# Performance work log

Measured on AMD Instinct MI355X. Metric: run time of the kernel, lower is better.

Reference implementation:

```python
import jax, jax.numpy as jnp
import numpy as np

EPS = 1e-9
LAMBDA_VIOLATION = 0.5

B, S, K, N, M = 2048, 20, 128, 256, 10  # batch, num_samples, k, n, m


def setup_inputs() -> dict:
    key = jax.random.key(0)
    k1, k2, k3, k4 = jax.random.split(key, 4)
    y_pred = jax.random.uniform(k1, (B, 1), dtype=jnp.float32) * 10.0 + 1.0
    y_true = jax.random.uniform(k2, (B, 1), dtype=jnp.float32) * 10.0 + 1.0
    P_padded = jax.random.normal(k3, (B, K, N - K), dtype=jnp.float32)
    samples = jax.random.normal(k4, (B, S, K), dtype=jnp.float32)
    return {"y_pred": y_pred, "y_true": y_true, "P_padded": P_padded,
            "samples": samples, "m": M}


def reference(y_pred, y_true, P_padded, samples, m):
    b, s, k = samples.shape
    n = k + P_padded.shape[2]
    # LogMSE term
    yp = jnp.clip(y_pred, EPS)
    yt = jnp.clip(y_true, EPS)
    logmse = jnp.mean((jnp.log2(yt) - jnp.log2(yp)) ** 2)
    # Build generator matrices G = [I_k | P] : [B, k, n]
    I = jnp.broadcast_to(jnp.eye(k, dtype=P_padded.dtype), (b, k, k))
    G = jnp.concatenate([I, P_padded], axis=2)
    # Random codewords: [B, S, n]
    codewords = jnp.einsum('bsk,bkn->bsn', samples, G)
    mags = jnp.abs(codewords).reshape(b * s, n)
    top_vals, _ = jax.lax.top_k(mags, m + 1)  # [B*S, m+1] descending
    hm = (top_vals[:, 0] / (top_vals[:, m] + EPS)).reshape(b, s)
    max_hm = jnp.max(hm, axis=1)  # [B]
    penalty = jnp.sum(jax.nn.relu(max_hm - y_pred.squeeze(-1)))
    violation = penalty / b
    total_loss = logmse + LAMBDA_VIOLATION * violation
    return total_loss, logmse, violation
```

## Files before the change

kernel.cpp:

```cpp
#include <hip/hip_runtime.h>
#include <math.h>

#define EPSF 1e-9f
#define KK 128
#define MTOP 10

__global__ __launch_bounds__(256, 4) void fused_kernel(
    const float* __restrict__ y_pred, const float* __restrict__ y_true,
    const float* __restrict__ P, const float* __restrict__ samples,
    float* __restrict__ partial )
{
    const int tid   = threadIdx.x;
    const int wave  = tid >> 6;
    const int lane  = tid & 63;
    const int b     = blockIdx.x;
    const int r0    = wave * 5;
    const int sg    = lane >> 5;
    const int c     = lane & 31;
    const int j4    = c << 2;
    const int kbase = sg << 6;

    const float* __restrict__ Pb = P + ((size_t)b << 14);
    const float* __restrict__ Sb = samples + (size_t)b * (20 * KK);

    __shared__ float sS[20 * KK];
    __shared__ float red[4];

#pragma unroll
    for (int i = 0; i < 5; ++i) {
        const int idx = (i * 256 + tid) * 2;
        *(float2*)&sS[idx] = *(const float2*)(Sb + idx);
    }
    __syncthreads();

    float4 acc[5];
#pragma unroll
    for (int r = 0; r < 5; ++r) acc[r] = make_float4(0.f, 0.f, 0.f, 0.f);

    const float* __restrict__ Pw = Pb + (size_t)kbase * KK + j4;
#pragma unroll 2
    for (int kk = 0; kk < 64; kk += 4) {
        float4 p0 = *(const float4*)(Pw + (kk + 0) * KK);
        float4 p1 = *(const float4*)(Pw + (kk + 1) * KK);
        float4 p2 = *(const float4*)(Pw + (kk + 2) * KK);
        float4 p3 = *(const float4*)(Pw + (kk + 3) * KK);
#pragma unroll
        for (int r = 0; r < 5; ++r) {
            float4 s = *(const float4*)&sS[(r0 + r) * KK + kbase + kk];
            acc[r].x = fmaf(s.x, p0.x, acc[r].x);
            acc[r].y = fmaf(s.x, p0.y, acc[r].y);
            acc[r].z = fmaf(s.x, p0.z, acc[r].z);
            acc[r].w = fmaf(s.x, p0.w, acc[r].w);
            acc[r].x = fmaf(s.y, p1.x, acc[r].x);
            acc[r].y = fmaf(s.y, p1.y, acc[r].y);
            acc[r].z = fmaf(s.y, p1.z, acc[r].z);
            acc[r].w = fmaf(s.y, p1.w, acc[r].w);
            acc[r].x = fmaf(s.z, p2.x, acc[r].x);
            acc[r].y = fmaf(s.z, p2.y, acc[r].y);
            acc[r].z = fmaf(s.z, p2.z, acc[r].z);
            acc[r].w = fmaf(s.z, p2.w, acc[r].w);
            acc[r].x = fmaf(s.w, p3.x, acc[r].x);
            acc[r].y = fmaf(s.w, p3.y, acc[r].y);
            acc[r].z = fmaf(s.w, p3.z, acc[r].z);
            acc[r].w = fmaf(s.w, p3.w, acc[r].w);
        }
    }

    float w0[5], w1[5], w2[5], w3[5];
#pragma unroll
    for (int r = 0; r < 5; ++r) {
        float ax = acc[r].x + __shfl_xor(acc[r].x, 32, 64);
        float ay = acc[r].y + __shfl_xor(acc[r].y, 32, 64);
        float az = acc[r].z + __shfl_xor(acc[r].z, 32, 64);
        float aw = acc[r].w + __shfl_xor(acc[r].w, 32, 64);
        float4 idv = *(const float4*)&sS[(r0 + r) * KK + j4];
        w0[r] = fabsf(sg ? idv.x : ax);
        w1[r] = fabsf(sg ? idv.y : ay);
        w2[r] = fabsf(sg ? idv.z : az);
        w3[r] = fabsf(sg ? idv.w : aw);
    }

    float mx[5];
#pragma unroll
    for (int r = 0; r < 5; ++r) {
        float lm = fmaxf(fmaxf(w0[r], w1[r]), fmaxf(w2[r], w3[r]));
#pragma unroll
        for (int d = 32; d >= 1; d >>= 1)
            lm = fmaxf(lm, __shfl_xor(lm, d, 64));
        mx[r] = lm;
    }

    unsigned lo[5], hi[5];
#pragma unroll
    for (int r = 0; r < 5; ++r) { lo[r] = 0u; hi[r] = __float_as_uint(mx[r]); }

    while (lo[0] < hi[0] || lo[1] < hi[1] || lo[2] < hi[2] ||
           lo[3] < hi[3] || lo[4] < hi[4]) {
#pragma unroll
        for (int r = 0; r < 5; ++r) {
            unsigned mid = lo[r] + ((hi[r] - lo[r] + 1u) >> 1);
            float mf = __uint_as_float(mid);
            int cnt = __popcll(__ballot(w0[r] > mf)) + __popcll(__ballot(w1[r] > mf))
                    + __popcll(__ballot(w2[r] > mf)) + __popcll(__ballot(w3[r] > mf));
            bool g = cnt >= (MTOP + 1);
            lo[r] = g ? mid : lo[r];
            hi[r] = g ? hi[r] : mid - 1u;
        }
    }

    float hmax = 0.f;
#pragma unroll
    for (int r = 0; r < 5; ++r) {
        float m11 = __uint_as_float(lo[r] + 1u);
        hmax = fmaxf(hmax, mx[r] / (m11 + EPSF));
    }

    if (lane == 0) red[wave] = hmax;
    __syncthreads();
    if (tid == 0) {
        float hb  = fmaxf(fmaxf(red[0], red[1]), fmaxf(red[2], red[3]));
        float ypv = y_pred[b];
        float yp  = fmaxf(ypv, EPSF);
        float yt  = fmaxf(y_true[b], EPSF);
        float d   = log2f(yt) - log2f(yp);
        partial[2 * b]     = d * d;
        partial[2 * b + 1] = fmaxf(hb - ypv, 0.f);
    }
}

__global__ __launch_bounds__(256) void finalize_kernel(
    const float* __restrict__ partial, float* __restrict__ out, float invB)
{
    const int t = threadIdx.x;
    float sl = 0.f, sp = 0.f;
#pragma unroll
    for (int i = 0; i < 8; ++i) {
        float2 v = *(const float2*)(partial + 2 * (t + i * 256));
        sl += v.x; sp += v.y;
    }
#pragma unroll
    for (int d = 32; d >= 1; d >>= 1) {
        sl += __shfl_xor(sl, d, 64);
        sp += __shfl_xor(sp, d, 64);
    }
    __shared__ float rl[4], rp[4];
    const int w = t >> 6;
    if ((t & 63) == 0) { rl[w] = sl; rp[w] = sp; }
    __syncthreads();
    if (t == 0) {
        float L = (rl[0] + rl[1] + rl[2] + rl[3]) * invB;
        float V = (rp[0] + rp[1] + rp[2] + rp[3]) * invB;
        out[0] = L + 0.5f * V;
        out[1] = L;
        out[2] = V;
    }
}

extern "C" void kernel_launch(void* const* d_in, const int* in_sizes, int n_in,
                              void* d_out, int out_size, void* d_ws, size_t ws_size,
                              hipStream_t stream) {
    const float* y_pred  = (const float*)d_in[0];
    const float* y_true  = (const float*)d_in[1];
    const float* P       = (const float*)d_in[2];
    const float* samples = (const float*)d_in[3];
    const int B = in_sizes[0];

    float* partial = (float*)d_ws;

    fused_kernel<<<B, 256, 0, stream>>>(y_pred, y_true, P, samples, partial);
    finalize_kernel<<<1, 256, 0, stream>>>(partial, (float*)d_out, 1.0f / (float)B);
}
```

Measured before the change: 235.9 us.

## Split each batch into two 128-thread blocks with swizzled mapping and prefetch

Each batch element is now handled by two 128-thread blocks, each doing 10 of the 20 sample rows, so the grid has twice as many smaller blocks. Block indices are swizzled so the two halves of a batch element land apart, and the P loads are software-prefetched one step ahead of the FMA loop. The log-MSE and penalty math moves into the finalize kernel, which also merges the two half maxima. The aim is better occupancy and latency hiding, but P for each batch is now read by two blocks, doubling its global traffic unless the cache serves it.

Result: slower. 260.0 us (+10.2%).

```diff
diff --git a/kernel.cpp b/kernel.cpp
--- a/kernel.cpp
+++ b/kernel.cpp
@@ -5,31 +5,39 @@
 #define KK 128
 #define MTOP 10
 
-__global__ __launch_bounds__(256, 4) void fused_kernel(
-    const float* __restrict__ y_pred, const float* __restrict__ y_true,
+__global__ __launch_bounds__(128, 7) void fused_kernel(
     const float* __restrict__ P, const float* __restrict__ samples,
-    float* __restrict__ partial )
+    float* __restrict__ hq )
 {
-    const int tid   = threadIdx.x;
-    const int wave  = tid >> 6;
-    const int lane  = tid & 63;
-    const int b     = blockIdx.x;
-    const int r0    = wave * 5;
-    const int sg    = lane >> 5;
-    const int c     = lane & 31;
-    const int j4    = c << 2;
+    const int tid  = threadIdx.x;
+    const int wave = tid >> 6;
+    const int lane = tid & 63;
+
+    const int u = blockIdx.x;
+    int b, h;
+    if ((gridDim.x & 15) == 0) {
+        const int perx = gridDim.x >> 4;
+        b = (u & 7) * perx + (u >> 4);
+        h = (u >> 3) & 1;
+    } else {
+        b = u >> 1;
+        h = u & 1;
+    }
+    const int q  = h * 2 + wave;
+    const int sg = lane >> 5;
+    const int c  = lane & 31;
+    const int j4 = c << 2;
     const int kbase = sg << 6;
 
-    const float* __restrict__ Pb = P + ((size_t)b << 14);
-    const float* __restrict__ Sb = samples + (size_t)b * (20 * KK);
+    __shared__ float sS[2 * 5 * KK];
+    __shared__ float redh[2];
+    float* __restrict__ sW = sS + wave * (5 * KK);
 
-    __shared__ float sS[20 * KK];
-    __shared__ float red[4];
-
+    const float* __restrict__ Sb = samples + ((size_t)b * 20 + q * 5) * KK;
 #pragma unroll
     for (int i = 0; i < 5; ++i) {
-        const int idx = (i * 256 + tid) * 2;
-        *(float2*)&sS[idx] = *(const float2*)(Sb + idx);
+        const int idx = i * KK + lane * 2;
+        *(float2*)&sW[idx] = *(const float2*)(Sb + idx);
     }
     __syncthreads();
 
@@ -37,16 +45,25 @@
 #pragma unroll
     for (int r = 0; r < 5; ++r) acc[r] = make_float4(0.f, 0.f, 0.f, 0.f);
 
-    const float* __restrict__ Pw = Pb + (size_t)kbase * KK + j4;
-#pragma unroll 2
+    const float* __restrict__ Pw = P + ((size_t)b << 14) + (size_t)kbase * KK + j4;
+    float4 p0 = *(const float4*)(Pw + 0 * KK);
+    float4 p1 = *(const float4*)(Pw + 1 * KK);
+    float4 p2 = *(const float4*)(Pw + 2 * KK);
+    float4 p3 = *(const float4*)(Pw + 3 * KK);
+#pragma unroll
     for (int kk = 0; kk < 64; kk += 4) {
-        float4 p0 = *(const float4*)(Pw + (kk + 0) * KK);
-        float4 p1 = *(const float4*)(Pw + (kk + 1) * KK);
-        float4 p2 = *(const float4*)(Pw + (kk + 2) * KK);
-        float4 p3 = *(const float4*)(Pw + (kk + 3) * KK);
+        float4 q0, q1, q2, q3;
+        const bool pf = (kk + 4) < 64;
+        if (pf) {
+            const float* Pn = Pw + (size_t)(kk + 4) * KK;
+            q0 = *(const float4*)(Pn + 0 * KK);
+            q1 = *(const float4*)(Pn + 1 * KK);
+            q2 = *(const float4*)(Pn + 2 * KK);
+            q3 = *(const float4*)(Pn + 3 * KK);
+        }
 #pragma unroll
         for (int r = 0; r < 5; ++r) {
-            float4 s = *(const float4*)&sS[(r0 + r) * KK + kbase + kk];
+            float4 s = *(const float4*)&sW[r * KK + kbase + kk];
             acc[r].x = fmaf(s.x, p0.x, acc[r].x);
             acc[r].y = fmaf(s.x, p0.y, acc[r].y);
             acc[r].z = fmaf(s.x, p0.z, acc[r].z);
@@ -64,6 +81,7 @@
             acc[r].z = fmaf(s.w, p3.z, acc[r].z);
             acc[r].w = fmaf(s.w, p3.w, acc[r].w);
         }
+        if (pf) { p0 = q0; p1 = q1; p2 = q2; p3 = q3; }
     }
 
     float w0[5], w1[5], w2[5], w3[5];
@@ -73,7 +91,7 @@
         float ay = acc[r].y + __shfl_xor(acc[r].y, 32, 64);
         float az = acc[r].z + __shfl_xor(acc[r].z, 32, 64);
         float aw = acc[r].w + __shfl_xor(acc[r].w, 32, 64);
-        float4 idv = *(const float4*)&sS[(r0 + r) * KK + j4];
+        float4 idv = *(const float4*)&sW[r * KK + j4];
         w0[r] = fabsf(sg ? idv.x : ax);
         w1[r] = fabsf(sg ? idv.y : ay);
         w2[r] = fabsf(sg ? idv.z : az);
@@ -115,28 +133,27 @@
         hmax = fmaxf(hmax, mx[r] / (m11 + EPSF));
     }
 
-    if (lane == 0) red[wave] = hmax;
+    if (lane == 0) redh[wave] = hmax;
     __syncthreads();
-    if (tid == 0) {
-        float hb  = fmaxf(fmaxf(red[0], red[1]), fmaxf(red[2], red[3]));
-        float ypv = y_pred[b];
-        float yp  = fmaxf(ypv, EPSF);
-        float yt  = fmaxf(y_true[b], EPSF);
-        float d   = log2f(yt) - log2f(yp);
-        partial[2 * b]     = d * d;
-        partial[2 * b + 1] = fmaxf(hb - ypv, 0.f);
-    }
+    if (tid == 0) hq[2 * b + h] = fmaxf(redh[0], redh[1]);
 }
 
 __global__ __launch_bounds__(256) void finalize_kernel(
-    const float* __restrict__ partial, float* __restrict__ out, float invB)
+    const float* __restrict__ hq, const float* __restrict__ y_pred,
+    const float* __restrict__ y_true, float* __restrict__ out,
+    float invB, int B)
 {
     const int t = threadIdx.x;
     float sl = 0.f, sp = 0.f;
-#pragma unroll
-    for (int i = 0; i < 8; ++i) {
-        float2 v = *(const float2*)(partial + 2 * (t + i * 256));
-        sl += v.x; sp += v.y;
+    for (int bb = t; bb < B; bb += 256) {
+        float2 h2 = *(const float2*)(hq + 2 * bb);
+        float hb  = fmaxf(h2.x, h2.y);
+        float ypv = y_pred[bb];
+        float yp  = fmaxf(ypv, EPSF);
+        float yt  = fmaxf(y_true[bb], EPSF);
+        float d   = log2f(yt) - log2f(yp);
+        sl += d * d;
+        sp += fmaxf(hb - ypv, 0.f);
     }
 #pragma unroll
     for (int d = 32; d >= 1; d >>= 1) {
@@ -165,8 +182,9 @@
     const float* samples = (const float*)d_in[3];
     const int B = in_sizes[0];
 
-    float* partial = (float*)d_ws;
+    float* hq = (float*)d_ws;
 
-    fused_kernel<<<B, 256, 0, stream>>>(y_pred, y_true, P, samples, partial);
-    finalize_kernel<<<1, 256, 0, stream>>>(partial, (float*)d_out, 1.0f / (float)B);
+    fused_kernel<<<2 * B, 128, 0, stream>>>(P, samples, hq);
+    finalize_kernel<<<1, 256, 0, stream>>>(hq, y_pred, y_true, (float*)d_out,
+                                           1.0f / (float)B, B);
 }
```

## Stage P through double-buffered LDS with async global_load_lds pipeline

Applied to the files above, without the earlier changes.

Replaces direct per-thread global loads of the P matrix with asynchronous global-to-LDS copies via global_load_lds into a two-stage shared buffer. Each of eight chunks is prefetched while the previous chunk is consumed, so memory latency overlaps the FMA work. The occupancy hint rises from 4 to 6 blocks per CU. The cost is 16 KB of extra LDS per block, a barrier per chunk, and correctness that depends on the async-copy lane-to-address mapping and on no wait for outstanding vmcnt before the barrier.

After: 232.1 us. About the same (-1.6%).

```diff
diff --git a/kernel.cpp b/kernel.cpp
--- a/kernel.cpp
+++ b/kernel.cpp
@@ -5,7 +5,48 @@
 #define KK 128
 #define MTOP 10
 
-__global__ __launch_bounds__(256, 4) void fused_kernel(
+
+#define GLDS16(G, L) __builtin_amdgcn_global_load_lds(                    \
+    (const __attribute__((address_space(1))) void*)(G),                   \
+    (__attribute__((address_space(3))) void*)(L), 16, 0, 0)
+
+#define STAGE_ISSUE(T, BUF, I)                                            \
+    GLDS16(Pb + (size_t)(((T) << 3) + rowoff + (wave << 2) + ((I) << 1)   \
+                         + l5) * KK + (lx << 2),                          \
+           &sP[BUF][((wave << 2) + ((I) << 1)) * KK])
+#define STAGE_CHUNK(T, BUF) { STAGE_ISSUE(T, BUF, 0); STAGE_ISSUE(T, BUF, 1); }
+
+#define FMA5G(T, BUF, G)                                                  \
+    {                                                                     \
+        const float* pbse = &sP[BUF][((sg << 3) + ((G) << 2)) * KK + j4]; \
+        float4 p0 = *(const float4*)(pbse + 0 * KK);                      \
+        float4 p1 = *(const float4*)(pbse + 1 * KK);                      \
+        float4 p2 = *(const float4*)(pbse + 2 * KK);                      \
+        float4 p3 = *(const float4*)(pbse + 3 * KK);                      \
+        const int soff = kbase + ((T) << 3) + ((G) << 2);                 \
+        _Pragma("unroll")                                                 \
+        for (int r = 0; r < 5; ++r) {                                     \
+            float4 s = *(const float4*)&sS[(r0 + r) * KK + soff];         \
+            acc[r].x = fmaf(s.x, p0.x, acc[r].x);                         \
+            acc[r].y = fmaf(s.x, p0.y, acc[r].y);                         \
+            acc[r].z = fmaf(s.x, p0.z, acc[r].z);                         \
+            acc[r].w = fmaf(s.x, p0.w, acc[r].w);                         \
+            acc[r].x = fmaf(s.y, p1.x, acc[r].x);                         \
+            acc[r].y = fmaf(s.y, p1.y, acc[r].y);                         \
+            acc[r].z = fmaf(s.y, p1.z, acc[r].z);                         \
+            acc[r].w = fmaf(s.y, p1.w, acc[r].w);                         \
+            acc[r].x = fmaf(s.z, p2.x, acc[r].x);                         \
+            acc[r].y = fmaf(s.z, p2.y, acc[r].y);                         \
+            acc[r].z = fmaf(s.z, p2.z, acc[r].z);                         \
+            acc[r].w = fmaf(s.z, p2.w, acc[r].w);                         \
+            acc[r].x = fmaf(s.w, p3.x, acc[r].x);                         \
+            acc[r].y = fmaf(s.w, p3.y, acc[r].y);                         \
+            acc[r].z = fmaf(s.w, p3.z, acc[r].z);                         \
+            acc[r].w = fmaf(s.w, p3.w, acc[r].w);                         \
+        }                                                                 \
+    }
+
+__global__ __launch_bounds__(256, 6) void fused_kernel(
     const float* __restrict__ y_pred, const float* __restrict__ y_true,
     const float* __restrict__ P, const float* __restrict__ samples,
     float* __restrict__ partial )
@@ -19,11 +60,15 @@
     const int c     = lane & 31;
     const int j4    = c << 2;
     const int kbase = sg << 6;
+    const int l5    = lane >> 5;
+    const int lx    = lane & 31;
+    const int rowoff = (wave >= 2) ? 56 : 0;
 
     const float* __restrict__ Pb = P + ((size_t)b << 14);
     const float* __restrict__ Sb = samples + (size_t)b * (20 * KK);
 
     __shared__ float sS[20 * KK];
+    __shared__ float sP[2][16 * KK];
     __shared__ float red[4];
 
 #pragma unroll
@@ -31,40 +76,25 @@
         const int idx = (i * 256 + tid) * 2;
         *(float2*)&sS[idx] = *(const float2*)(Sb + idx);
     }
+
+    float4 acc[5];
+#pragma unroll
+    for (int r = 0; r < 5; ++r) acc[r] = make_float4(0.f, 0.f, 0.f, 0.f);
+
+    STAGE_CHUNK(0, 0);
     __syncthreads();
 
-    float4 acc[5];
-#pragma unroll
-    for (int r = 0; r < 5; ++r) acc[r] = make_float4(0.f, 0.f, 0.f, 0.f);
-
-    const float* __restrict__ Pw = Pb + (size_t)kbase * KK + j4;
-#pragma unroll 2
-    for (int kk = 0; kk < 64; kk += 4) {
-        float4 p0 = *(const float4*)(Pw + (kk + 0) * KK);
-        float4 p1 = *(const float4*)(Pw + (kk + 1) * KK);
-        float4 p2 = *(const float4*)(Pw + (kk + 2) * KK);
-        float4 p3 = *(const float4*)(Pw + (kk + 3) * KK);
-#pragma unroll
-        for (int r = 0; r < 5; ++r) {
-            float4 s = *(const float4*)&sS[(r0 + r) * KK + kbase + kk];
-            acc[r].x = fmaf(s.x, p0.x, acc[r].x);
-            acc[r].y = fmaf(s.x, p0.y, acc[r].y);
-            acc[r].z = fmaf(s.x, p0.z, acc[r].z);
-            acc[r].w = fmaf(s.x, p0.w, acc[r].w);
-            acc[r].x = fmaf(s.y, p1.x, acc[r].x);
-            acc[r].y = fmaf(s.y, p1.y, acc[r].y);
-            acc[r].z = fmaf(s.y, p1.z, acc[r].z);
-            acc[r].w = fmaf(s.y, p1.w, acc[r].w);
-            acc[r].x = fmaf(s.z, p2.x, acc[r].x);
-            acc[r].y = fmaf(s.z, p2.y, acc[r].y);
-            acc[r].z = fmaf(s.z, p2.z, acc[r].z);
-            acc[r].w = fmaf(s.z, p2.w, acc[r].w);
-            acc[r].x = fmaf(s.w, p3.x, acc[r].x);
-            acc[r].y = fmaf(s.w, p3.y, acc[r].y);
-            acc[r].z = fmaf(s.w, p3.z, acc[r].z);
-            acc[r].w = fmaf(s.w, p3.w, acc[r].w);
-        }
-    }
+    int cur = 0;
+#pragma unroll 1
+    for (int t = 0; t < 7; ++t) {
+        STAGE_CHUNK(t + 1, cur ^ 1);
+        FMA5G(t, cur, 0)
+        FMA5G(t, cur, 1)
+        __syncthreads();
+        cur ^= 1;
+    }
+    FMA5G(7, cur, 0)
+    FMA5G(7, cur, 1)
 
     float w0[5], w1[5], w2[5], w3[5];
 #pragma unroll
```

## Double-buffer P tiles into LDS via async global_load_lds and early-exit top-k search

Applied to the files above, without the earlier changes.

The P matrix is now streamed through a double-buffered LDS tile using direct global-to-LDS loads, overlapping the next chunk's fetch with FMAs on the current one. Samples are read straight from global memory as wave-uniform addresses instead of being staged in LDS, and each lane computes two output columns over the full k, which removes the cross-half shuffle reduction. The bisection for the 11th-largest value now exits early when exactly 10 elements exceed the midpoint, taking the max of the rest directly. Occupancy hint is raised to 8 blocks, which adds register pressure and block-wide barriers per chunk.

After: 264.0 us. +11.9%, slower.

```diff
diff --git a/kernel.cpp b/kernel.cpp
--- a/kernel.cpp
+++ b/kernel.cpp
@@ -5,79 +5,108 @@
 #define KK 128
 #define MTOP 10
 
-__global__ __launch_bounds__(256, 4) void fused_kernel(
+
+#define GLDS16(G, L) __builtin_amdgcn_global_load_lds(                    \
+    (const __attribute__((address_space(1))) void*)(G),                   \
+    (__attribute__((address_space(3))) void*)(L), 16, 0, 0)
+
+#define STAGE(T, BUF)                                                     \
+    { GLDS16(Pb + (size_t)((T) * 16 + 4 * wave + 0 + l5) * KK + (lx << 2),\
+             &sP[BUF][(4 * wave + 0) * KK]);                              \
+      GLDS16(Pb + (size_t)((T) * 16 + 4 * wave + 2 + l5) * KK + (lx << 2),\
+             &sP[BUF][(4 * wave + 2) * KK]); }
+
+#define SUBCHUNK(BUFP, T, H, A0, A1)                                      \
+    {                                                                     \
+        const float* __restrict__ pb = (BUFP) + (H) * 8 * KK + j2;        \
+        float2 p0 = *(const float2*)(pb + 0 * KK);                        \
+        float2 p1 = *(const float2*)(pb + 1 * KK);                        \
+        float2 p2 = *(const float2*)(pb + 2 * KK);                        \
+        float2 p3 = *(const float2*)(pb + 3 * KK);                        \
+        float2 p4 = *(const float2*)(pb + 4 * KK);                        \
+        float2 p5 = *(const float2*)(pb + 5 * KK);                        \
+        float2 p6 = *(const float2*)(pb + 6 * KK);                        \
+        float2 p7 = *(const float2*)(pb + 7 * KK);                        \
+        _Pragma("unroll")                                                 \
+        for (int r = 0; r < 5; ++r) {                                     \
+            const float* __restrict__ su = Su + r * KK + (T) * 16 + (H) * 8; \
+            float4 sA = *(const float4*)(su);                             \
+            float4 sB = *(const float4*)(su + 4);                         \
+            A0[r] = fmaf(sA.x, p0.x, A0[r]); A1[r] = fmaf(sA.x, p0.y, A1[r]); \
+            A0[r] = fmaf(sA.y, p1.x, A0[r]); A1[r] = fmaf(sA.y, p1.y, A1[r]); \
+            A0[r] = fmaf(sA.z, p2.x, A0[r]); A1[r] = fmaf(sA.z, p2.y, A1[r]); \
+            A0[r] = fmaf(sA.w, p3.x, A0[r]); A1[r] = fmaf(sA.w, p3.y, A1[r]); \
+            A0[r] = fmaf(sB.x, p4.x, A0[r]); A1[r] = fmaf(sB.x, p4.y, A1[r]); \
+            A0[r] = fmaf(sB.y, p5.x, A0[r]); A1[r] = fmaf(sB.y, p5.y, A1[r]); \
+            A0[r] = fmaf(sB.z, p6.x, A0[r]); A1[r] = fmaf(sB.z, p6.y, A1[r]); \
+            A0[r] = fmaf(sB.w, p7.x, A0[r]); A1[r] = fmaf(sB.w, p7.y, A1[r]); \
+        }                                                                 \
+    }
+
+__global__ __launch_bounds__(256, 8) void fused_kernel(
     const float* __restrict__ y_pred, const float* __restrict__ y_true,
     const float* __restrict__ P, const float* __restrict__ samples,
     float* __restrict__ partial )
 {
-    const int tid   = threadIdx.x;
-    const int wave  = tid >> 6;
-    const int lane  = tid & 63;
-    const int b     = blockIdx.x;
-    const int r0    = wave * 5;
-    const int sg    = lane >> 5;
-    const int c     = lane & 31;
-    const int j4    = c << 2;
-    const int kbase = sg << 6;
+    const int tid  = threadIdx.x;
+    const int wave = tid >> 6;
+    const int lane = tid & 63;
+    const int b    = blockIdx.x;
+    const int r0   = wave * 5;
+    const int j2   = lane << 1;
+    const int l5   = lane >> 5;
+    const int lx   = lane & 31;
 
     const float* __restrict__ Pb = P + ((size_t)b << 14);
     const float* __restrict__ Sb = samples + (size_t)b * (20 * KK);
-
-    __shared__ float sS[20 * KK];
+    const int ru = __builtin_amdgcn_readfirstlane(r0);
+    const float* __restrict__ Su = Sb + (size_t)ru * KK;
+
+    __shared__ float sP[2][16 * KK];
     __shared__ float red[4];
 
-#pragma unroll
-    for (int i = 0; i < 5; ++i) {
-        const int idx = (i * 256 + tid) * 2;
-        *(float2*)&sS[idx] = *(const float2*)(Sb + idx);
-    }
+    float accL0[5], accL1[5], accH0[5], accH1[5];
+#pragma unroll
+    for (int r = 0; r < 5; ++r) {
+        accL0[r] = 0.f; accL1[r] = 0.f; accH0[r] = 0.f; accH1[r] = 0.f;
+    }
+
+    STAGE(0, 0);
     __syncthreads();
 
-    float4 acc[5];
-#pragma unroll
-    for (int r = 0; r < 5; ++r) acc[r] = make_float4(0.f, 0.f, 0.f, 0.f);
-
-    const float* __restrict__ Pw = Pb + (size_t)kbase * KK + j4;
-#pragma unroll 2
-    for (int kk = 0; kk < 64; kk += 4) {
-        float4 p0 = *(const float4*)(Pw + (kk + 0) * KK);
-        float4 p1 = *(const float4*)(Pw + (kk + 1) * KK);
-        float4 p2 = *(const float4*)(Pw + (kk + 2) * KK);
-        float4 p3 = *(const float4*)(Pw + (kk + 3) * KK);
-#pragma unroll
-        for (int r = 0; r < 5; ++r) {
-            float4 s = *(const float4*)&sS[(r0 + r) * KK + kbase + kk];
-            acc[r].x = fmaf(s.x, p0.x, acc[r].x);
-            acc[r].y = fmaf(s.x, p0.y, acc[r].y);
-            acc[r].z = fmaf(s.x, p0.z, acc[r].z);
-            acc[r].w = fmaf(s.x, p0.w, acc[r].w);
-            acc[r].x = fmaf(s.y, p1.x, acc[r].x);
-            acc[r].y = fmaf(s.y, p1.y, acc[r].y);
-            acc[r].z = fmaf(s.y, p1.z, acc[r].z);
-            acc[r].w = fmaf(s.y, p1.w, acc[r].w);
-            acc[r].x = fmaf(s.z, p2.x, acc[r].x);
-            acc[r].y = fmaf(s.z, p2.y, acc[r].y);
-            acc[r].z = fmaf(s.z, p2.z, acc[r].z);
-            acc[r].w = fmaf(s.z, p2.w, acc[r].w);
-            acc[r].x = fmaf(s.w, p3.x, acc[r].x);
-            acc[r].y = fmaf(s.w, p3.y, acc[r].y);
-            acc[r].z = fmaf(s.w, p3.z, acc[r].z);
-            acc[r].w = fmaf(s.w, p3.w, acc[r].w);
-        }
+    int cur = 0;
+#pragma unroll 1
+    for (int t = 0; t < 4; ++t) {
+        STAGE(t + 1, cur ^ 1);
+        const float* __restrict__ bufp = &sP[0][0] + cur * (16 * KK);
+        SUBCHUNK(bufp, t, 0, accL0, accL1)
+        SUBCHUNK(bufp, t, 1, accL0, accL1)
+        __syncthreads();
+        cur ^= 1;
+    }
+#pragma unroll 1
+    for (int t = 4; t < 7; ++t) {
+        STAGE(t + 1, cur ^ 1);
+        const float* __restrict__ bufp = &sP[0][0] + cur * (16 * KK);
+        SUBCHUNK(bufp, t, 0, accH0, accH1)
+        SUBCHUNK(bufp, t, 1, accH0, accH1)
+        __syncthreads();
+        cur ^= 1;
+    }
+    {
+        const float* __restrict__ bufp = &sP[0][0] + cur * (16 * KK);
+        SUBCHUNK(bufp, 7, 0, accH0, accH1)
+        SUBCHUNK(bufp, 7, 1, accH0, accH1)
     }
 
     float w0[5], w1[5], w2[5], w3[5];
 #pragma unroll
     for (int r = 0; r < 5; ++r) {
-        float ax = acc[r].x + __shfl_xor(acc[r].x, 32, 64);
-        float ay = acc[r].y + __shfl_xor(acc[r].y, 32, 64);
-        float az = acc[r].z + __shfl_xor(acc[r].z, 32, 64);
-        float aw = acc[r].w + __shfl_xor(acc[r].w, 32, 64);
-        float4 idv = *(const float4*)&sS[(r0 + r) * KK + j4];
-        w0[r] = fabsf(sg ? idv.x : ax);
-        w1[r] = fabsf(sg ? idv.y : ay);
-        w2[r] = fabsf(sg ? idv.z : az);
-        w3[r] = fabsf(sg ? idv.w : aw);
+        float2 sid = *(const float2*)(Sb + (size_t)(r0 + r) * KK + j2);
+        w0[r] = fabsf(accL0[r] + accH0[r]);
+        w1[r] = fabsf(accL1[r] + accH1[r]);
+        w2[r] = fabsf(sid.x);
+        w3[r] = fabsf(sid.y);
     }
 
     float mx[5];
@@ -91,27 +120,47 @@
     }
 
     unsigned lo[5], hi[5];
-#pragma unroll
-    for (int r = 0; r < 5; ++r) { lo[r] = 0u; hi[r] = __float_as_uint(mx[r]); }
-
-    while (lo[0] < hi[0] || lo[1] < hi[1] || lo[2] < hi[2] ||
-           lo[3] < hi[3] || lo[4] < hi[4]) {
+    float m11v[5];
+    int act[5];
+#pragma unroll
+    for (int r = 0; r < 5; ++r) {
+        lo[r] = 0u; hi[r] = __float_as_uint(mx[r]); m11v[r] = 0.f; act[r] = 1;
+    }
+
+    while ((act[0] && lo[0] < hi[0]) || (act[1] && lo[1] < hi[1]) ||
+           (act[2] && lo[2] < hi[2]) || (act[3] && lo[3] < hi[3]) ||
+           (act[4] && lo[4] < hi[4])) {
 #pragma unroll
         for (int r = 0; r < 5; ++r) {
-            unsigned mid = lo[r] + ((hi[r] - lo[r] + 1u) >> 1);
-            float mf = __uint_as_float(mid);
-            int cnt = __popcll(__ballot(w0[r] > mf)) + __popcll(__ballot(w1[r] > mf))
-                    + __popcll(__ballot(w2[r] > mf)) + __popcll(__ballot(w3[r] > mf));
-            bool g = cnt >= (MTOP + 1);
-            lo[r] = g ? mid : lo[r];
-            hi[r] = g ? hi[r] : mid - 1u;
+            if (act[r] && lo[r] < hi[r]) {
+                unsigned mid = lo[r] + ((hi[r] - lo[r] + 1u) >> 1);
+                float mf = __uint_as_float(mid);
+                int cnt = __popcll(__ballot(w0[r] > mf)) + __popcll(__ballot(w1[r] > mf))
+                        + __popcll(__ballot(w2[r] > mf)) + __popcll(__ballot(w3[r] > mf));
+                if (cnt == MTOP) {
+                    float t0 = (w0[r] <= mf) ? w0[r] : 0.f;
+                    float t1 = (w1[r] <= mf) ? w1[r] : 0.f;
+                    float t2 = (w2[r] <= mf) ? w2[r] : 0.f;
+                    float t3 = (w3[r] <= mf) ? w3[r] : 0.f;
+                    float lm = fmaxf(fmaxf(t0, t1), fmaxf(t2, t3));
+#pragma unroll
+                    for (int d = 32; d >= 1; d >>= 1)
+                        lm = fmaxf(lm, __shfl_xor(lm, d, 64));
+                    m11v[r] = lm;
+                    act[r] = 0;
+                } else {
+                    bool g = cnt >= (MTOP + 1);
+                    lo[r] = g ? mid : lo[r];
+                    hi[r] = g ? hi[r] : mid - 1u;
+                }
+            }
         }
     }
 
     float hmax = 0.f;
 #pragma unroll
     for (int r = 0; r < 5; ++r) {
-        float m11 = __uint_as_float(lo[r] + 1u);
+        float m11 = act[r] ? __uint_as_float(lo[r] + 1u) : m11v[r];
         hmax = fmaxf(hmax, mx[r] / (m11 + EPSF));
     }
 
```
